# Kernel optimization log

Hardware: AMD Instinct MI355X
Metric: run time of the kernel (lower is better)

## Reference

```python
import jax, jax.numpy as jnp
import numpy as np

B, H, W, C = 2, 48, 96, 128
N = H * W
NH, HD = 8, 32
WIN_R = 1
WLEN = 2 * WIN_R + 2
ATTN_NUM = WLEN * WLEN
FIELD_DIM = 2
D_SELF = C + FIELD_DIM + NH * 2   # 146
E_SELF = D_SELF + 1               # 147 (noc embed)
D_CROSS = C + FIELD_DIM           # 130
ATTN_DIM = NH * HD                # 256
HID = C * 2                       # ConvGLU hidden
SCALE = HD ** -0.5


def init_coords():
    gx, gy = jnp.meshgrid(jnp.arange(W, dtype=jnp.float32), jnp.arange(H, dtype=jnp.float32))
    return jnp.stack([gx, gy], axis=-1)[None]  # [1,H,W,2] (x,y)


def layer_norm(x, g, b, eps=1e-5):
    mu = x.mean(-1, keepdims=True)
    var = ((x - mu) ** 2).mean(-1, keepdims=True)
    return (x - mu) * jax.lax.rsqrt(var + eps) * g + b


def swap_halves(t):
    a, b = jnp.split(t, 2, axis=0)
    return jnp.concatenate([b, a], axis=0)


def bilinear_sample(img, coords):
    # img [B,H,W,C]; coords [B,H,W,2] absolute (x,y)
    x = jnp.clip(coords[..., 0], 0.0, W - 1.0)
    y = jnp.clip(coords[..., 1], 0.0, H - 1.0)
    x0 = jnp.clip(jnp.floor(x), 0, W - 2).astype(jnp.int32); x1 = x0 + 1
    y0 = jnp.clip(jnp.floor(y), 0, H - 2).astype(jnp.int32); y1 = y0 + 1
    wx = (x - x0)[..., None]; wy = (y - y0)[..., None]
    bi = jnp.arange(img.shape[0])[:, None, None]
    v00 = img[bi, y0, x0]; v01 = img[bi, y0, x1]
    v10 = img[bi, y1, x0]; v11 = img[bi, y1, x1]
    return (1 - wy) * ((1 - wx) * v00 + wx * v01) + wy * ((1 - wx) * v10 + wx * v11)


def consistency_mask(field, A=2.0):
    offset = field + init_coords()
    f_t2r = bilinear_sample(swap_halves(field), offset)
    diff = jnp.abs(field + f_t2r).sum(-1, keepdims=True)
    return (diff < A).astype(field.dtype)  # [B,H,W,1]


def match_attention_core(q, k, v, max_offset):
    # q,k,v: [B,N,NH,HD]; max_offset: [B,N,NH,2] absolute (x,y)
    r = WIN_R
    ox = jnp.clip(max_offset[..., 0], float(r), W - 1 - r - 0.001)
    oy = jnp.clip(max_offset[..., 1], float(r), H - 1 - r - 0.001)
    mxf = jnp.floor(ox); myf = jnp.floor(oy)
    fx = (ox - mxf).transpose(0, 2, 1)[..., None, None]  # [B,NH,N,1,1]
    fy = (oy - myf).transpose(0, 2, 1)[..., None, None]
    mx = mxf.astype(jnp.int32).transpose(0, 2, 1)  # [B,NH,N]
    my = myf.astype(jnp.int32).transpose(0, 2, 1)
    qh = q.transpose(0, 2, 1, 3); kh = k.transpose(0, 2, 1, 3); vh = v.transpose(0, 2, 1, 3)
    dxs = jnp.arange(WLEN) - r                    # window: floor-r .. floor+r+1
    gx = mx[..., None] + dxs                      # [B,NH,N,WLEN]
    gy = my[..., None] + dxs
    idx = (gy[..., :, None] * W + gx[..., None, :]).reshape(B, NH, N, ATTN_NUM)
    bi = jnp.arange(B)[:, None, None, None]
    hi = jnp.arange(NH)[None, :, None, None]
    kg = kh[bi, hi, idx]                          # [B,NH,N,ATTN_NUM,HD]
    s = jnp.einsum('bhnd,bhnad->bhna', qh, kg) * SCALE
    S = s.reshape(B, NH, N, WLEN, WLEN)           # [..., y, x]
    w00 = (1 - fy) * (1 - fx); w01 = (1 - fy) * fx; w10 = fy * (1 - fx); w11 = fy * fx
    # continuous (2r+1)^2 window scores by bilinear interp of integer-grid scores
    s_cont = (w00 * S[..., :-1, :-1] + w01 * S[..., :-1, 1:]
              + w10 * S[..., 1:, :-1] + w11 * S[..., 1:, 1:])
    p = jax.nn.softmax(s_cont.reshape(B, NH, N, -1), axis=-1).reshape(s_cont.shape)
    # scatter continuous probs back to the (2r+2)^2 integer grid with bilinear weights
    Ag = jnp.zeros((B, NH, N, WLEN, WLEN), p.dtype)
    Ag = Ag.at[..., :-1, :-1].add(w00 * p)
    Ag = Ag.at[..., :-1, 1:].add(w01 * p)
    Ag = Ag.at[..., 1:, :-1].add(w10 * p)
    Ag = Ag.at[..., 1:, 1:].add(w11 * p)
    Af = Ag.reshape(B, NH, N, ATTN_NUM)
    vg = vh[bi, hi, idx]                          # [B,NH,N,ATTN_NUM,HD]
    out = jnp.einsum('bhna,bhnad->bhnd', Af, vg)
    return out.transpose(0, 2, 1, 3).reshape(B, N, ATTN_DIM), Af.transpose(0, 2, 1, 3)


def reference(x, self_rpos, field, field_scale, n0_g, n0_b, n1_g, n1_b, n2_g, n2_b,
              sq_w, sk_w, sv_w, sp_w, cq_w, ck_w, cv_w, cg_w, cp_w,
              fc1_w, fc1_b, dw_w, dw_b, fc2_w, fc2_b):
    noc = consistency_mask(jax.lax.stop_gradient(field))
    xc = jnp.concatenate([x, field * field_scale, self_rpos], axis=-1)  # [B,H,W,D_SELF]
    coords0 = jnp.tile(init_coords(), (1, 1, 1, NH))  # [1,H,W,2*NH]
    self_off = (self_rpos + coords0).reshape(B, N, NH, 2)
    # --- self MatchAttention (noc_embed) ---
    h0 = layer_norm(xc, n0_g, n0_b).reshape(B, N, D_SELF)
    xe = jnp.concatenate([h0, noc.reshape(B, N, 1)], axis=-1)
    q = (xe @ sq_w).reshape(B, N, NH, HD)
    k = (xe @ sk_w).reshape(B, N, NH, HD)
    v = (xe @ sv_w).reshape(B, N, NH, HD)
    o, _ = match_attention_core(q, k, v, self_off)
    xc = xc + (o @ sp_w).reshape(B, H, W, D_SELF)
    self_rpos_out = xc[..., -NH * 2:]
    xc = xc[..., :D_CROSS]
    xc = xc.at[..., -1].set(0.0)  # stereo: zero y-flow
    field1 = xc[..., -FIELD_DIM:] / field_scale
    off = (jnp.tile(field1, (1, 1, 1, NH)) + coords0).reshape(B, N, NH, 2)
    # --- cross MatchAttention ---
    h1 = layer_norm(xc, n1_g, n1_b).reshape(B, N, D_CROSS)
    ref = h1
    tgt = swap_halves(h1)
    g = jax.nn.silu(ref @ cg_w)
    q = (ref @ cq_w).reshape(B, N, NH, HD)
    k = (tgt @ ck_w).reshape(B, N, NH, HD)
    v = (tgt @ cv_w).reshape(B, N, NH, HD)
    o, attn = match_attention_core(q, k, v, off)
    o = jnp.concatenate([g * o, attn.reshape(B, N, NH * ATTN_NUM)], axis=-1)
    xc = xc + (o @ cp_w).reshape(B, H, W, D_CROSS)
    xc = xc.at[..., -1].set(0.0)
    field2 = xc[..., -FIELD_DIM:] / field_scale
    xo = xc[..., :C]
    # --- ConvGLU MLP ---
    h2 = layer_norm(xo, n2_g, n2_b)
    u = h2 @ fc1_w + fc1_b
    a, gv = jnp.split(u, 2, axis=-1)
    a = jax.lax.conv_general_dilated(a, dw_w, (1, 1), 'SAME',
                                     dimension_numbers=('NHWC', 'HWIO', 'NHWC'),
                                     feature_group_count=HID) + dw_b
    a = jax.nn.gelu(a, approximate=False) * gv
    xo = xo + (a @ fc2_w + fc2_b)
    return xo, self_rpos_out, field2


def setup_inputs() -> dict:
    key = jax.random.key(0)
    ks = jax.random.split(key, 16)
    def rn(i, shape, s=1.0):
        return jax.random.normal(ks[i], shape, dtype=jnp.float32) * s
    return {
        'x': rn(0, (B, H, W, C)),
        'self_rpos': rn(1, (B, H, W, NH * 2)),
        'field': rn(2, (B, H, W, FIELD_DIM)),
        'field_scale': 0.1 * jnp.ones((1, 1, 1, 2), jnp.float32),
        'n0_g': jnp.ones((D_SELF,), jnp.float32), 'n0_b': jnp.zeros((D_SELF,), jnp.float32),
        'n1_g': jnp.ones((D_CROSS,), jnp.float32), 'n1_b': jnp.zeros((D_CROSS,), jnp.float32),
        'n2_g': jnp.ones((C,), jnp.float32), 'n2_b': jnp.zeros((C,), jnp.float32),
        'sq_w': rn(3, (E_SELF, ATTN_DIM), 0.02), 'sk_w': rn(4, (E_SELF, ATTN_DIM), 0.02),
        'sv_w': rn(5, (E_SELF, ATTN_DIM), 0.02), 'sp_w': rn(6, (ATTN_DIM, D_SELF), 0.02),
        'cq_w': rn(7, (D_CROSS, ATTN_DIM), 0.02), 'ck_w': rn(8, (D_CROSS, ATTN_DIM), 0.02),
        'cv_w': rn(9, (D_CROSS, ATTN_DIM), 0.02), 'cg_w': rn(10, (D_CROSS, ATTN_DIM), 0.02),
        'cp_w': rn(11, (ATTN_DIM + NH * ATTN_NUM, D_CROSS), 0.02),
        'fc1_w': rn(12, (C, 2 * HID), 0.02), 'fc1_b': jnp.zeros((2 * HID,), jnp.float32),
        'dw_w': rn(13, (3, 3, 1, HID), 0.1), 'dw_b': jnp.zeros((HID,), jnp.float32),
        'fc2_w': rn(14, (HID, C), 0.02), 'fc2_b': jnp.zeros((C,), jnp.float32),
    }
```

## Files before the change

### kernel.cpp

```cpp
#include <hip/hip_runtime.h>
#include <math.h>

namespace {
constexpr int Bn = 2, Hh = 48, Ww = 96, Cch = 128;
constexpr int Nn = Hh * Ww;
constexpr int NHh = 8;
constexpr int DSELF = 146, ESELF = 147, DCROSS = 130;
constexpr int Mrows = Bn * Nn;
constexpr float SCALEf = 0.17677669529663687f;
}

typedef float f32x4 __attribute__((ext_vector_type(4)));
typedef short s16x8 __attribute__((ext_vector_type(8)));

__device__ __forceinline__ unsigned short f2b(float f) {
  unsigned int u = __float_as_uint(f);
  u = u + 0x7fffu + ((u >> 16) & 1u);
  return (unsigned short)(u >> 16);
}
__device__ __forceinline__ float b2f(unsigned short u) {
  return __uint_as_float((unsigned int)u << 16);
}

__device__ __forceinline__ f32x4 mfma_bf16(s16x8 a, s16x8 b, f32x4 c) {
  f32x4 d;
  asm volatile("v_mfma_f32_16x16x32_bf16 %0, %1, %2, %3"
               : "=&v"(d) : "v"(a), "v"(b), "v"(c));
  return d;
}

__device__ __forceinline__ float wave_bcast_sum(float v) {
#pragma unroll
  for (int off = 32; off > 0; off >>= 1) v += __shfl_down(v, off);
  return __shfl(v, 0);
}

struct WDesc { const float* src; int K, N, Kp, dstOff, blkOff; };
struct WPack { WDesc d[11]; };

__device__ __forceinline__ void convert_w_body(const WPack& p, unsigned short* dst,
                                               int bi) {
  int mi = 0;
#pragma unroll
  for (int i = 1; i < 11; i++) if (bi >= p.d[i].blkOff) mi = i;
  WDesc w = p.d[mi];
  int e = (bi - w.blkOff) * 2048 + threadIdx.x * 8;
  int total = w.N * w.Kp;
  if (e >= total) return;
  int n = e / w.Kp, k0 = e - n * w.Kp;
  s16x8 pack;
#pragma unroll
  for (int j = 0; j < 8; j++) {
    int kk = k0 + j;
    float vv = (kk < w.K) ? w.src[(size_t)kk * w.N + n] : 0.f;
    pack[j] = (short)f2b(vv);
  }
  *reinterpret_cast<s16x8*>(dst + w.dstOff + e) = pack;
}

__global__ __launch_bounds__(256) void mfma_gemm_kernel(
    const unsigned short* __restrict__ A, int Kp,
    const unsigned short* __restrict__ Wt, int N,
    const float* __restrict__ bias, const float* __restrict__ resid,
    void* __restrict__ out, int swapA, int act, int out_bf16) {
  __shared__ unsigned short As[64 * 40];
  __shared__ unsigned short Bs[64 * 40];
  int tid = threadIdx.x;
  int m0 = blockIdx.y * 64, n0 = blockIdx.x * 64;
  int lane = tid & 63, wv = tid >> 6;
  int wr = wv >> 1, wc = wv & 1;
  int lr = lane & 15, lk = (lane >> 4) * 8;
  int sr = tid >> 2, sk8 = (tid & 3) * 8;
  int am = m0 + sr;
  if (swapA) am = (am < Mrows / 2) ? am + Mrows / 2 : am - Mrows / 2;
  const unsigned short* aptr = A + (size_t)am * Kp + sk8;
  int bn = n0 + sr;
  const unsigned short* bptr = (bn < N) ? Wt + (size_t)bn * Kp + sk8 : nullptr;
  f32x4 acc00 = {}, acc01 = {}, acc10 = {}, acc11 = {};
  for (int k0 = 0; k0 < Kp; k0 += 32) {
    s16x8 av = *reinterpret_cast<const s16x8*>(aptr + k0);
    s16x8 bv = {};
    if (bptr) bv = *reinterpret_cast<const s16x8*>(bptr + k0);
    *reinterpret_cast<s16x8*>(&As[sr * 40 + sk8]) = av;
    *reinterpret_cast<s16x8*>(&Bs[sr * 40 + sk8]) = bv;
    __syncthreads();
    s16x8 a0 = *reinterpret_cast<const s16x8*>(&As[(wr * 32 + lr) * 40 + lk]);
    s16x8 a1 = *reinterpret_cast<const s16x8*>(&As[(wr * 32 + 16 + lr) * 40 + lk]);
    s16x8 b0 = *reinterpret_cast<const s16x8*>(&Bs[(wc * 32 + lr) * 40 + lk]);
    s16x8 b1 = *reinterpret_cast<const s16x8*>(&Bs[(wc * 32 + 16 + lr) * 40 + lk]);
    acc00 = mfma_bf16(a0, b0, acc00);
    acc01 = mfma_bf16(a0, b1, acc01);
    acc10 = mfma_bf16(a1, b0, acc10);
    acc11 = mfma_bf16(a1, b1, acc11);
    __syncthreads();
  }
  int rowBase = m0 + wr * 32 + (lane >> 4) * 4;
  f32x4 accs[2][2] = {{acc00, acc01}, {acc10, acc11}};
#pragma unroll
  for (int fc = 0; fc < 2; fc++) {
    int col = n0 + wc * 32 + fc * 16 + lr;
    if (col >= N) continue;
    float bval = bias ? bias[col] : 0.f;
    bool dosilu = (act == 1) || (act == 2 && col >= 256);
#pragma unroll
    for (int fr = 0; fr < 2; fr++) {
#pragma unroll
      for (int r = 0; r < 4; r++) {
        int row = rowBase + fr * 16 + r;
        float vv = accs[fr][fc][r] + bval;
        if (resid) vv += resid[(size_t)row * N + col];
        if (dosilu) vv = vv / (1.f + expf(-vv));
        if (out_bf16)
          ((unsigned short*)out)[(size_t)row * N + col] = f2b(vv);
        else
          ((float*)out)[(size_t)row * N + col] = vv;
      }
    }
  }
}

__global__ __launch_bounds__(128) void mfma_gemm32_kernel(
    const unsigned short* __restrict__ A, int Kp,
    const unsigned short* __restrict__ Wt, int N,
    const float* __restrict__ bias, const float* __restrict__ resid,
    void* __restrict__ out, int swapA, int act, int out_bf16) {
  __shared__ unsigned short As[32 * 40];
  __shared__ unsigned short Bs[64 * 40];
  int tid = threadIdx.x;
  int m0 = blockIdx.y * 32, n0 = blockIdx.x * 64;
  int lane = tid & 63, wv = tid >> 6;
  int lr = lane & 15, lk = (lane >> 4) * 8;
  int sr = tid >> 2, sk8 = (tid & 3) * 8;
  int am = m0 + sr;
  if (swapA) am = (am < Mrows / 2) ? am + Mrows / 2 : am - Mrows / 2;
  const unsigned short* aptr = A + (size_t)am * Kp + sk8;
  int bn0 = n0 + sr, bn1 = n0 + sr + 32;
  const unsigned short* bptr0 = (bn0 < N) ? Wt + (size_t)bn0 * Kp + sk8 : nullptr;
  const unsigned short* bptr1 = (bn1 < N) ? Wt + (size_t)bn1 * Kp + sk8 : nullptr;
  f32x4 acc00 = {}, acc01 = {}, acc10 = {}, acc11 = {};
  for (int k0 = 0; k0 < Kp; k0 += 32) {
    s16x8 av = *reinterpret_cast<const s16x8*>(aptr + k0);
    s16x8 bv0 = {}, bv1 = {};
    if (bptr0) bv0 = *reinterpret_cast<const s16x8*>(bptr0 + k0);
    if (bptr1) bv1 = *reinterpret_cast<const s16x8*>(bptr1 + k0);
    *reinterpret_cast<s16x8*>(&As[sr * 40 + sk8]) = av;
    *reinterpret_cast<s16x8*>(&Bs[sr * 40 + sk8]) = bv0;
    *reinterpret_cast<s16x8*>(&Bs[(sr + 32) * 40 + sk8]) = bv1;
    __syncthreads();
    s16x8 a0 = *reinterpret_cast<const s16x8*>(&As[lr * 40 + lk]);
    s16x8 a1 = *reinterpret_cast<const s16x8*>(&As[(16 + lr) * 40 + lk]);
    s16x8 b0 = *reinterpret_cast<const s16x8*>(&Bs[(wv * 32 + lr) * 40 + lk]);
    s16x8 b1 = *reinterpret_cast<const s16x8*>(&Bs[(wv * 32 + 16 + lr) * 40 + lk]);
    acc00 = mfma_bf16(a0, b0, acc00);
    acc01 = mfma_bf16(a0, b1, acc01);
    acc10 = mfma_bf16(a1, b0, acc10);
    acc11 = mfma_bf16(a1, b1, acc11);
    __syncthreads();
  }
  int rowBase = m0 + (lane >> 4) * 4;
  f32x4 accs[2][2] = {{acc00, acc01}, {acc10, acc11}};
#pragma unroll
  for (int fc = 0; fc < 2; fc++) {
    int col = n0 + wv * 32 + fc * 16 + lr;
    if (col >= N) continue;
    float bval = bias ? bias[col] : 0.f;
    bool dosilu = (act == 1) || (act == 2 && col >= 256);
#pragma unroll
    for (int fr = 0; fr < 2; fr++) {
#pragma unroll
      for (int r = 0; r < 4; r++) {
        int row = rowBase + fr * 16 + r;
        float vv = accs[fr][fc][r] + bval;
        if (resid) vv += resid[(size_t)row * N + col];
        if (dosilu) vv = vv / (1.f + expf(-vv));
        if (out_bf16)
          ((unsigned short*)out)[(size_t)row * N + col] = f2b(vv);
        else
          ((float*)out)[(size_t)row * N + col] = vv;
      }
    }
  }
}

__global__ __launch_bounds__(256) void prep_kernel(
    WPack wp, unsigned short* __restrict__ warena, int nconv,
    const float* __restrict__ x, const float* __restrict__ rpos,
    const float* __restrict__ field, const float* __restrict__ fs,
    const float* __restrict__ n0g, const float* __restrict__ n0b,
    float* __restrict__ xc, unsigned short* __restrict__ xe_b) {
  if (blockIdx.x < (unsigned)nconv) {
    convert_w_body(wp, warena, blockIdx.x);
    return;
  }
  int wv = threadIdx.x >> 6, lane = threadIdx.x & 63;
  int pix = (blockIdx.x - nconv) * 4 + wv;
  int b = pix / Nn, n = pix - b * Nn;
  int py = n / Ww, px = n - py * Ww;
  const float* xrow = x + (size_t)pix * Cch;
  const float* rrow = rpos + (size_t)pix * 16;
  float f0 = field[(size_t)pix * 2 + 0], f1 = field[(size_t)pix * 2 + 1];
  float fsx = fs[0], fsy = fs[1];
  float vals[3];
#pragma unroll
  for (int i = 0; i < 3; i++) {
    int c = lane + i * 64;
    float v = 0.f;
    if (c < Cch) v = xrow[c];
    else if (c == 128) v = f0 * fsx;
    else if (c == 129) v = f1 * fsy;
    else if (c < DSELF) v = rrow[c - 130];
    vals[i] = v;
  }
  float* xcrow = xc + (size_t)pix * DSELF;
#pragma unroll
  for (int i = 0; i < 3; i++) {
    int c = lane + i * 64;
    if (c < DSELF) xcrow[c] = vals[i];
  }
  float s = 0.f;
#pragma unroll
  for (int i = 0; i < 3; i++) { int c = lane + i * 64; if (c < DSELF) s += vals[i]; }
  float mu = wave_bcast_sum(s) * (1.f / DSELF);
  float s2 = 0.f;
#pragma unroll
  for (int i = 0; i < 3; i++) {
    int c = lane + i * 64;
    if (c < DSELF) { float d = vals[i] - mu; s2 += d * d; }
  }
  float var = wave_bcast_sum(s2) * (1.f / DSELF);
  float rs = rsqrtf(var + 1e-5f);
  float noc = 0.f;
  if (lane == 0) {
    float ox = fminf(fmaxf(f0 + (float)px, 0.f), (float)(Ww - 1));
    float oy = fminf(fmaxf(f1 + (float)py, 0.f), (float)(Hh - 1));
    float x0f = fminf(fmaxf(floorf(ox), 0.f), (float)(Ww - 2));
    float y0f = fminf(fmaxf(floorf(oy), 0.f), (float)(Hh - 2));
    int x0 = (int)x0f, y0 = (int)y0f;
    float wx = ox - x0f, wy = oy - y0f;
    const float* fo = field + (size_t)(1 - b) * Nn * 2;
    const float* p00 = fo + ((size_t)y0 * Ww + x0) * 2;
    const float* p10 = fo + ((size_t)(y0 + 1) * Ww + x0) * 2;
    float v0 = (1.f - wy) * ((1.f - wx) * p00[0] + wx * p00[2]) +
               wy * ((1.f - wx) * p10[0] + wx * p10[2]);
    float v1 = (1.f - wy) * ((1.f - wx) * p00[1] + wx * p00[3]) +
               wy * ((1.f - wx) * p10[1] + wx * p10[3]);
    float diff = fabsf(f0 + v0) + fabsf(f1 + v1);
    noc = (diff < 2.f) ? 1.f : 0.f;
  }
  noc = __shfl(noc, 0);
  unsigned short* xerow = xe_b + (size_t)pix * 160;
#pragma unroll
  for (int i = 0; i < 3; i++) {
    int c = lane + i * 64;
    if (c < 160) {
      float v;
      if (c < DSELF) v = (vals[i] - mu) * rs * n0g[c] + n0b[c];
      else if (c == 146) v = noc;
      else v = 0.f;
      xerow[c] = f2b(v);
    }
  }
}

__global__ __launch_bounds__(256) void attn_wave_kernel(
    const float* __restrict__ qbuf, int qstride, int gOff,
    const float* __restrict__ kvbuf, int kvstride, int koff, int voff,
    const float* __restrict__ rpos, const float* __restrict__ xc2,
    const float* __restrict__ fs, unsigned short* __restrict__ o, int o_stride,
    int mode) {
  int wv = threadIdx.x >> 6, lane = threadIdx.x & 63;
  int pix = blockIdx.x * 4 + wv;
  int b = pix / Nn, n = pix - b * Nn;
  int py = n / Ww, px = n - py * Ww;
  int h = lane >> 3, c = lane & 7;
  size_t row = (size_t)pix;
  float ox, oy;
  if (mode == 0) {
    ox = rpos[row * 16 + 2 * h] + (float)px;
    oy = rpos[row * 16 + 2 * h + 1] + (float)py;
  } else {
    ox = xc2[row * DCROSS + 128] / fs[0] + (float)px;
    oy = (float)py;
  }
  ox = fminf(fmaxf(ox, 1.0f), 93.999f);
  oy = fminf(fmaxf(oy, 1.0f), 45.999f);
  float mxf = floorf(ox), myf = floorf(oy);
  float fx = ox - mxf, fy = oy - myf;
  int mx = (int)mxf, my = (int)myf;
  int base = b * Nn;

  float4 qv = *reinterpret_cast<const float4*>(qbuf + row * qstride + lane * 4);
  float s[16];
#pragma unroll
  for (int j = 0; j < 4; j++) {
    int gy = my - 1 + j;
#pragma unroll
    for (int i = 0; i < 4; i++) {
      int gx = mx - 1 + i;
      int idx = gy * Ww + gx;
      float4 kv = *reinterpret_cast<const float4*>(
          kvbuf + (size_t)(base + idx) * kvstride + koff + lane * 4);
      float d = qv.x * kv.x + qv.y * kv.y + qv.z * kv.z + qv.w * kv.w;
      d += __shfl_xor(d, 1);
      d += __shfl_xor(d, 2);
      d += __shfl_xor(d, 4);
      s[j * 4 + i] = d * SCALEf;
    }
  }
  float w00 = (1.f - fy) * (1.f - fx), w01 = (1.f - fy) * fx;
  float w10 = fy * (1.f - fx), w11 = fy * fx;
  float sc[9];
#pragma unroll
  for (int j = 0; j < 3; j++)
#pragma unroll
    for (int i = 0; i < 3; i++)
      sc[j * 3 + i] = w00 * s[j * 4 + i] + w01 * s[j * 4 + i + 1] +
                      w10 * s[(j + 1) * 4 + i] + w11 * s[(j + 1) * 4 + i + 1];
  float mval = sc[0];
#pragma unroll
  for (int i = 1; i < 9; i++) mval = fmaxf(mval, sc[i]);
  float p[9], psum = 0.f;
#pragma unroll
  for (int i = 0; i < 9; i++) { p[i] = expf(sc[i] - mval); psum += p[i]; }
  float inv = 1.f / psum;
#pragma unroll
  for (int i = 0; i < 9; i++) p[i] *= inv;
  float Ag[16] = {};
#pragma unroll
  for (int j = 0; j < 3; j++)
#pragma unroll
    for (int i = 0; i < 3; i++) {
      float pv = p[j * 3 + i];
      Ag[j * 4 + i] += w00 * pv;
      Ag[j * 4 + i + 1] += w01 * pv;
      Ag[(j + 1) * 4 + i] += w10 * pv;
      Ag[(j + 1) * 4 + i + 1] += w11 * pv;
    }
  float4 acc = make_float4(0.f, 0.f, 0.f, 0.f);
#pragma unroll
  for (int j = 0; j < 4; j++) {
    int gy = my - 1 + j;
#pragma unroll
    for (int i = 0; i < 4; i++) {
      int gx = mx - 1 + i;
      int idx = gy * Ww + gx;
      float4 vv = *reinterpret_cast<const float4*>(
          kvbuf + (size_t)(base + idx) * kvstride + voff + lane * 4);
      float w = Ag[j * 4 + i];
      acc.x += w * vv.x; acc.y += w * vv.y; acc.z += w * vv.z; acc.w += w * vv.w;
    }
  }
  if (gOff >= 0) {
    float4 gg = *reinterpret_cast<const float4*>(qbuf + row * qstride + gOff + lane * 4);
    acc.x *= gg.x; acc.y *= gg.y; acc.z *= gg.z; acc.w *= gg.w;
  }
  unsigned int p0 = (unsigned int)f2b(acc.x) | ((unsigned int)f2b(acc.y) << 16);
  unsigned int p1 = (unsigned int)f2b(acc.z) | ((unsigned int)f2b(acc.w) << 16);
  *reinterpret_cast<uint2*>(o + row * o_stride + lane * 4) = make_uint2(p0, p1);
  if (mode == 1) {
    float a0 = 0.f, a1 = 0.f;
#pragma unroll
    for (int a = 0; a < 8; a++) {
      if (c == a) { a0 = Ag[2 * a]; a1 = Ag[2 * a + 1]; }
    }
    unsigned int pa = (unsigned int)f2b(a0) | ((unsigned int)f2b(a1) << 16);
    *reinterpret_cast<unsigned int*>(o + row * o_stride + 256 + h * 16 + 2 * c) = pa;
  }
}

__global__ __launch_bounds__(256) void post_self_kernel(
    const float* __restrict__ xcn, const float* __restrict__ n1g,
    const float* __restrict__ n1b, float* __restrict__ out_rpos,
    float* __restrict__ xc2, unsigned short* __restrict__ h1_b) {
  int wv = threadIdx.x >> 6, lane = threadIdx.x & 63;
  int pix = blockIdx.x * 4 + wv;
  const float* row = xcn + (size_t)pix * DSELF;
  float vals[3];
#pragma unroll
  for (int i = 0; i < 3; i++) {
    int c = lane + i * 64;
    vals[i] = (c < DSELF) ? row[c] : 0.f;
  }
#pragma unroll
  for (int i = 0; i < 3; i++) {
    int c = lane + i * 64;
    if (c >= 130 && c < 146) out_rpos[(size_t)pix * 16 + (c - 130)] = vals[i];
  }
#pragma unroll
  for (int i = 0; i < 3; i++) {
    int c = lane + i * 64;
    if (c == 129) vals[i] = 0.f;
  }
  float* x2row = xc2 + (size_t)pix * DCROSS;
#pragma unroll
  for (int i = 0; i < 3; i++) {
    int c = lane + i * 64;
    if (c < DCROSS) x2row[c] = vals[i];
  }
  float s = 0.f;
#pragma unroll
  for (int i = 0; i < 3; i++) { int c = lane + i * 64; if (c < DCROSS) s += vals[i]; }
  float mu = wave_bcast_sum(s) * (1.f / DCROSS);
  float s2 = 0.f;
#pragma unroll
  for (int i = 0; i < 3; i++) {
    int c = lane + i * 64;
    if (c < DCROSS) { float d = vals[i] - mu; s2 += d * d; }
  }
  float var = wave_bcast_sum(s2) * (1.f / DCROSS);
  float rs = rsqrtf(var + 1e-5f);
  unsigned short* h1row = h1_b + (size_t)pix * 160;
#pragma unroll
  for (int i = 0; i < 3; i++) {
    int c = lane + i * 64;
    if (c < 160) {
      float v = (c < DCROSS) ? (vals[i] - mu) * rs * n1g[c] + n1b[c] : 0.f;
      h1row[c] = f2b(v);
    }
  }
}

__global__ __launch_bounds__(256) void post_cross_kernel(
    const float* __restrict__ xc2n, const float* __restrict__ fs,
    const float* __restrict__ n2g, const float* __restrict__ n2b,
    float* __restrict__ out_f2, float* __restrict__ xob,
    unsigned short* __restrict__ h2_b) {
  int wv = threadIdx.x >> 6, lane = threadIdx.x & 63;
  int pix = blockIdx.x * 4 + wv;
  const float* row = xc2n + (size_t)pix * DCROSS;
  float vals[3];
#pragma unroll
  for (int i = 0; i < 3; i++) {
    int c = lane + i * 64;
    vals[i] = (c < DCROSS) ? row[c] : 0.f;
  }
  if (lane == 0) out_f2[(size_t)pix * 2 + 0] = vals[2] / fs[0];
  if (lane == 1) out_f2[(size_t)pix * 2 + 1] = 0.f;
  float* xrow = xob + (size_t)pix * Cch;
#pragma unroll
  for (int i = 0; i < 2; i++) {
    int c = lane + i * 64;
    xrow[c] = vals[i];
  }
  float s = vals[0] + vals[1];
  float mu = wave_bcast_sum(s) * (1.f / Cch);
  float d0 = vals[0] - mu, d1 = vals[1] - mu;
  float var = wave_bcast_sum(d0 * d0 + d1 * d1) * (1.f / Cch);
  float rs = rsqrtf(var + 1e-5f);
  unsigned short* h2row = h2_b + (size_t)pix * Cch;
#pragma unroll
  for (int i = 0; i < 2; i++) {
    int c = lane + i * 64;
    h2row[c] = f2b((vals[i] - mu) * rs * n2g[c] + n2b[c]);
  }
}

__global__ __launch_bounds__(256) void dwconv_kernel(
    const unsigned short* __restrict__ ub, const float* __restrict__ dww,
    const float* __restrict__ dwb, unsigned short* __restrict__ aout) {
  int t = blockIdx.x * 256 + threadIdx.x;
  int c8 = (t & 31) * 8;
  int pix = t >> 5;
  int b = pix / Nn, n = pix - b * Nn;
  int py = n / Ww, px = n - py * Ww;
  float acc[8];
#pragma unroll
  for (int j = 0; j < 8; j++) acc[j] = dwb[c8 + j];
#pragma unroll
  for (int ky = 0; ky < 3; ky++) {
    int yy = py + ky - 1;
    if (yy < 0 || yy >= Hh) continue;
#pragma unroll
    for (int kx = 0; kx < 3; kx++) {
      int xx = px + kx - 1;
      if (xx < 0 || xx >= Ww) continue;
      s16x8 uv = *reinterpret_cast<const s16x8*>(
          ub + ((size_t)(b * Nn + yy * Ww + xx)) * 512 + c8);
      const float* wrow = dww + (ky * 3 + kx) * 256 + c8;
#pragma unroll
      for (int j = 0; j < 8; j++)
        acc[j] += b2f((unsigned short)uv[j]) * wrow[j];
    }
  }
  s16x8 gate = *reinterpret_cast<const s16x8*>(ub + (size_t)pix * 512 + 256 + c8);
  s16x8 outp;
#pragma unroll
  for (int j = 0; j < 8; j++) {
    float a = acc[j];
    float ge = 0.5f * a * (1.f + erff(a * 0.70710678118654752f));
    outp[j] = (short)f2b(ge * b2f((unsigned short)gate[j]));
  }
  *reinterpret_cast<s16x8*>(aout + (size_t)pix * 256 + c8) = outp;
}

extern "C" void kernel_launch(void* const* d_in, const int* in_sizes, int n_in,
                              void* d_out, int out_size, void* d_ws, size_t ws_size,
                              hipStream_t stream) {
  (void)in_sizes; (void)n_in; (void)out_size; (void)ws_size;
  const float* x    = (const float*)d_in[0];
  const float* rpos = (const float*)d_in[1];
  const float* field= (const float*)d_in[2];
  const float* fs   = (const float*)d_in[3];
  const float* n0g  = (const float*)d_in[4];
  const float* n0b  = (const float*)d_in[5];
  const float* n1g  = (const float*)d_in[6];
  const float* n1b  = (const float*)d_in[7];
  const float* n2g  = (const float*)d_in[8];
  const float* n2b  = (const float*)d_in[9];
  const float* sq_w = (const float*)d_in[10];
  const float* sk_w = (const float*)d_in[11];
  const float* sv_w = (const float*)d_in[12];
  const float* sp_w = (const float*)d_in[13];
  const float* cq_w = (const float*)d_in[14];
  const float* ck_w = (const float*)d_in[15];
  const float* cv_w = (const float*)d_in[16];
  const float* cg_w = (const float*)d_in[17];
  const float* cp_w = (const float*)d_in[18];
  const float* fc1w = (const float*)d_in[19];
  const float* fc1b = (const float*)d_in[20];
  const float* dww  = (const float*)d_in[21];
  const float* dwb  = (const float*)d_in[22];
  const float* fc2w = (const float*)d_in[23];
  const float* fc2b = (const float*)d_in[24];

  float* ws = (float*)d_ws;
  float* xc    = ws + 0;
  float* xcn   = ws + 1345536;
  float* xc2   = ws + 2691072;
  float* xc2n  = ws + 3889152;
  float* xob   = ws + 5087232;
  unsigned short* xe_b   = (unsigned short*)(ws + 6266880);
  unsigned short* h1_b   = (unsigned short*)(ws + 7004160);
  unsigned short* h2_b   = (unsigned short*)(ws + 7741440);
  float* qkv   = ws + 8331264;
  float* qg    = ws + 15409152;
  float* kv    = ws + 20127744;
  unsigned short* o_b    = (unsigned short*)(ws + 24846336);
  unsigned short* ocat_b = (unsigned short*)(ws + 26025984);
  unsigned short* warena = (unsigned short*)(ws + 27795456);
  unsigned short* u_b    = (unsigned short*)qkv;
  unsigned short* aconv_b = o_b;

  float* out_xo   = (float*)d_out;
  float* out_rpos = out_xo + 1179648;
  float* out_f2   = out_xo + 1327104;

  const int oSQKV = 0;
  const int oSP   = 122880;
  const int oCQG  = 160256;
  const int oCKV  = 242176;
  const int oCP   = 324096;
  const int oF1   = 374016;
  const int oF2   = 439552;
  WPack wp;
  auto setw = [&](int i, const float* src, int K, int N, int Kp, int off) {
    wp.d[i].src = src; wp.d[i].K = K; wp.d[i].N = N; wp.d[i].Kp = Kp;
    wp.d[i].dstOff = off;
  };
  setw(0, sq_w, 147, 256, 160, oSQKV);
  setw(1, sk_w, 147, 256, 160, oSQKV + 40960);
  setw(2, sv_w, 147, 256, 160, oSQKV + 81920);
  setw(3, sp_w, 256, 146, 256, oSP);
  setw(4, cq_w, 130, 256, 160, oCQG);
  setw(5, cg_w, 130, 256, 160, oCQG + 40960);
  setw(6, ck_w, 130, 256, 160, oCKV);
  setw(7, cv_w, 130, 256, 160, oCKV + 40960);
  setw(8, cp_w, 384, 130, 384, oCP);
  setw(9, fc1w, 128, 512, 128, oF1);
  setw(10, fc2w, 256, 128, 256, oF2);
  int nblk = 0;
  for (int i = 0; i < 11; i++) {
    wp.d[i].blkOff = nblk;
    nblk += (wp.d[i].N * wp.d[i].Kp + 2047) / 2048;
  }

  dim3 blk(256);
  auto gemm = [&](const unsigned short* A, int Kp, int woff, int N,
                  const float* bias, const float* resid, void* out,
                  int swapA, int act, int obf) {
    if (N <= 384) {
      dim3 grid((N + 63) / 64, Mrows / 32);
      mfma_gemm32_kernel<<<grid, dim3(128), 0, stream>>>(
          A, Kp, warena + woff, N, bias, resid, out, swapA, act, obf);
    } else {
      dim3 grid((N + 63) / 64, Mrows / 64);
      mfma_gemm_kernel<<<grid, blk, 0, stream>>>(
          A, Kp, warena + woff, N, bias, resid, out, swapA, act, obf);
    }
  };

  prep_kernel<<<nblk + 2304, blk, 0, stream>>>(wp, warena, nblk, x, rpos, field,
                                               fs, n0g, n0b, xc, xe_b);
  gemm(xe_b, 160, oSQKV, 768, nullptr, nullptr, qkv, 0, 0, 0);
  attn_wave_kernel<<<2304, blk, 0, stream>>>(qkv, 768, -1, qkv, 768, 256, 512,
                                             rpos, nullptr, fs, o_b, 256, 0);
  gemm(o_b, 256, oSP, 146, nullptr, xc, xcn, 0, 0, 0);
  post_self_kernel<<<2304, blk, 0, stream>>>(xcn, n1g, n1b, out_rpos, xc2, h1_b);
  gemm(h1_b, 160, oCQG, 512, nullptr, nullptr, qg, 0, 2, 0);
  gemm(h1_b, 160, oCKV, 512, nullptr, nullptr, kv, 1, 0, 0);
  attn_wave_kernel<<<2304, blk, 0, stream>>>(qg, 512, 256, kv, 512, 0, 256,
                                             nullptr, xc2, fs, ocat_b, 384, 1);
  gemm(ocat_b, 384, oCP, 130, nullptr, xc2, xc2n, 0, 0, 0);
  post_cross_kernel<<<2304, blk, 0, stream>>>(xc2n, fs, n2g, n2b, out_f2, xob, h2_b);
  gemm(h2_b, 128, oF1, 512, fc1b, nullptr, u_b, 0, 0, 1);
  dwconv_kernel<<<1152, blk, 0, stream>>>(u_b, dww, dwb, aconv_b);
  gemm(aconv_b, 256, oF2, 128, fc2b, xob, out_xo, 0, 0, 0);
}
```

Before: 160.9 us.

## Store attention K/V in fp16 and merge cross Q/G and K/V GEMMs

Measured after the change: 147.7 us, median of 2. 8.2% less time.

```diff
diff --git a/kernel.cpp b/kernel.cpp
--- a/kernel.cpp
+++ b/kernel.cpp
@@ -12,6 +12,7 @@
 
 typedef float f32x4 __attribute__((ext_vector_type(4)));
 typedef short s16x8 __attribute__((ext_vector_type(8)));
+typedef _Float16 h16x4 __attribute__((ext_vector_type(4)));
 
 __device__ __forceinline__ unsigned short f2b(float f) {
   unsigned int u = __float_as_uint(f);
@@ -20,6 +21,10 @@
 }
 __device__ __forceinline__ float b2f(unsigned short u) {
   return __uint_as_float((unsigned int)u << 16);
+}
+__device__ __forceinline__ float4 ld4h(const _Float16* p) {
+  h16x4 h = *reinterpret_cast<const h16x4*>(p);
+  return make_float4((float)h[0], (float)h[1], (float)h[2], (float)h[3]);
 }
 
 __device__ __forceinline__ f32x4 mfma_bf16(s16x8 a, s16x8 b, f32x4 c) {
@@ -58,11 +63,31 @@
   *reinterpret_cast<s16x8*>(dst + w.dstOff + e) = pack;
 }
 
+__device__ __forceinline__ void gemm_store(
+    float vv, int row, int col, int N, int colSplit,
+    const float* __restrict__ bias, const float* __restrict__ resid,
+    void* __restrict__ out0, void* __restrict__ out1, int mode0, int act) {
+  if (bias) vv += bias[col];
+  if (act == 1 || (act == 3 && col >= 256 && col < 512))
+    vv = vv / (1.f + expf(-vv));
+  if (col < colSplit) {
+    if (resid) vv += resid[(size_t)row * colSplit + col];
+    if (mode0)
+      ((unsigned short*)out0)[(size_t)row * colSplit + col] = f2b(vv);
+    else
+      ((float*)out0)[(size_t)row * colSplit + col] = vv;
+  } else {
+    ((_Float16*)out1)[(size_t)row * (N - colSplit) + (col - colSplit)] =
+        (_Float16)vv;
+  }
+}
+
 __global__ __launch_bounds__(256) void mfma_gemm_kernel(
     const unsigned short* __restrict__ A, int Kp,
     const unsigned short* __restrict__ Wt, int N,
     const float* __restrict__ bias, const float* __restrict__ resid,
-    void* __restrict__ out, int swapA, int act, int out_bf16) {
+    void* __restrict__ out0, void* __restrict__ out1, int colSplit,
+    int mode0, int swapMode, int act) {
   __shared__ unsigned short As[64 * 40];
   __shared__ unsigned short Bs[64 * 40];
   int tid = threadIdx.x;
@@ -72,7 +97,8 @@
   int lr = lane & 15, lk = (lane >> 4) * 8;
   int sr = tid >> 2, sk8 = (tid & 3) * 8;
   int am = m0 + sr;
-  if (swapA) am = (am < Mrows / 2) ? am + Mrows / 2 : am - Mrows / 2;
+  int swp = (swapMode == 1) || (swapMode == 2 && n0 >= colSplit);
+  if (swp) am = (am < Mrows / 2) ? am + Mrows / 2 : am - Mrows / 2;
   const unsigned short* aptr = A + (size_t)am * Kp + sk8;
   int bn = n0 + sr;
   const unsigned short* bptr = (bn < N) ? Wt + (size_t)bn * Kp + sk8 : nullptr;
@@ -100,20 +126,13 @@
   for (int fc = 0; fc < 2; fc++) {
     int col = n0 + wc * 32 + fc * 16 + lr;
     if (col >= N) continue;
-    float bval = bias ? bias[col] : 0.f;
-    bool dosilu = (act == 1) || (act == 2 && col >= 256);
 #pragma unroll
     for (int fr = 0; fr < 2; fr++) {
 #pragma unroll
       for (int r = 0; r < 4; r++) {
         int row = rowBase + fr * 16 + r;
-        float vv = accs[fr][fc][r] + bval;
-        if (resid) vv += resid[(size_t)row * N + col];
-        if (dosilu) vv = vv / (1.f + expf(-vv));
-        if (out_bf16)
-          ((unsigned short*)out)[(size_t)row * N + col] = f2b(vv);
-        else
-          ((float*)out)[(size_t)row * N + col] = vv;
+        gemm_store(accs[fr][fc][r], row, col, N, colSplit, bias, resid,
+                   out0, out1, mode0, act);
       }
     }
   }
@@ -123,7 +142,8 @@
     const unsigned short* __restrict__ A, int Kp,
     const unsigned short* __restrict__ Wt, int N,
     const float* __restrict__ bias, const float* __restrict__ resid,
-    void* __restrict__ out, int swapA, int act, int out_bf16) {
+    void* __restrict__ out0, void* __restrict__ out1, int colSplit,
+    int mode0, int swapMode, int act) {
   __shared__ unsigned short As[32 * 40];
   __shared__ unsigned short Bs[64 * 40];
   int tid = threadIdx.x;
@@ -132,7 +152,8 @@
   int lr = lane & 15, lk = (lane >> 4) * 8;
   int sr = tid >> 2, sk8 = (tid & 3) * 8;
   int am = m0 + sr;
-  if (swapA) am = (am < Mrows / 2) ? am + Mrows / 2 : am - Mrows / 2;
+  int swp = (swapMode == 1) || (swapMode == 2 && n0 >= colSplit);
+  if (swp) am = (am < Mrows / 2) ? am + Mrows / 2 : am - Mrows / 2;
   const unsigned short* aptr = A + (size_t)am * Kp + sk8;
   int bn0 = n0 + sr, bn1 = n0 + sr + 32;
   const unsigned short* bptr0 = (bn0 < N) ? Wt + (size_t)bn0 * Kp + sk8 : nullptr;
@@ -163,20 +184,13 @@
   for (int fc = 0; fc < 2; fc++) {
     int col = n0 + wv * 32 + fc * 16 + lr;
     if (col >= N) continue;
-    float bval = bias ? bias[col] : 0.f;
-    bool dosilu = (act == 1) || (act == 2 && col >= 256);
 #pragma unroll
     for (int fr = 0; fr < 2; fr++) {
 #pragma unroll
       for (int r = 0; r < 4; r++) {
         int row = rowBase + fr * 16 + r;
-        float vv = accs[fr][fc][r] + bval;
-        if (resid) vv += resid[(size_t)row * N + col];
-        if (dosilu) vv = vv / (1.f + expf(-vv));
-        if (out_bf16)
-          ((unsigned short*)out)[(size_t)row * N + col] = f2b(vv);
-        else
-          ((float*)out)[(size_t)row * N + col] = vv;
+        gemm_store(accs[fr][fc][r], row, col, N, colSplit, bias, resid,
+                   out0, out1, mode0, act);
       }
     }
   }
@@ -264,7 +278,7 @@
 
 __global__ __launch_bounds__(256) void attn_wave_kernel(
     const float* __restrict__ qbuf, int qstride, int gOff,
-    const float* __restrict__ kvbuf, int kvstride, int koff, int voff,
+    const _Float16* __restrict__ kvbuf,
     const float* __restrict__ rpos, const float* __restrict__ xc2,
     const float* __restrict__ fs, unsigned short* __restrict__ o, int o_stride,
     int mode) {
@@ -298,8 +312,7 @@
     for (int i = 0; i < 4; i++) {
       int gx = mx - 1 + i;
       int idx = gy * Ww + gx;
-      float4 kv = *reinterpret_cast<const float4*>(
-          kvbuf + (size_t)(base + idx) * kvstride + koff + lane * 4);
+      float4 kv = ld4h(kvbuf + (size_t)(base + idx) * 512 + lane * 4);
       float d = qv.x * kv.x + qv.y * kv.y + qv.z * kv.z + qv.w * kv.w;
       d += __shfl_xor(d, 1);
       d += __shfl_xor(d, 2);
@@ -344,8 +357,7 @@
     for (int i = 0; i < 4; i++) {
       int gx = mx - 1 + i;
       int idx = gy * Ww + gx;
-      float4 vv = *reinterpret_cast<const float4*>(
-          kvbuf + (size_t)(base + idx) * kvstride + voff + lane * 4);
+      float4 vv = ld4h(kvbuf + (size_t)(base + idx) * 512 + 256 + lane * 4);
       float w = Ag[j * 4 + i];
       acc.x += w * vv.x; acc.y += w * vv.y; acc.z += w * vv.z; acc.w += w * vv.w;
     }
@@ -529,16 +541,16 @@
   float* xc2   = ws + 2691072;
   float* xc2n  = ws + 3889152;
   float* xob   = ws + 5087232;
-  unsigned short* xe_b   = (unsigned short*)(ws + 6266880);
-  unsigned short* h1_b   = (unsigned short*)(ws + 7004160);
-  unsigned short* h2_b   = (unsigned short*)(ws + 7741440);
-  float* qkv   = ws + 8331264;
-  float* qg    = ws + 15409152;
-  float* kv    = ws + 20127744;
-  unsigned short* o_b    = (unsigned short*)(ws + 24846336);
-  unsigned short* ocat_b = (unsigned short*)(ws + 26025984);
-  unsigned short* warena = (unsigned short*)(ws + 27795456);
-  unsigned short* u_b    = (unsigned short*)qkv;
+  unsigned short* xe_b = (unsigned short*)(ws + 6266880);
+  unsigned short* h1_b = (unsigned short*)(ws + 7004160);
+  unsigned short* h2_b = (unsigned short*)(ws + 7741440);
+  float* q32   = ws + 8331264;
+  _Float16* kv16 = (_Float16*)(ws + 10690560);
+  float* qg    = ws + 13049856;
+  unsigned short* o_b    = (unsigned short*)(ws + 17768448);
+  unsigned short* ocat_b = (unsigned short*)(ws + 18948096);
+  unsigned short* warena = (unsigned short*)(ws + 20717568);
+  unsigned short* u_b    = (unsigned short*)qg;
   unsigned short* aconv_b = o_b;
 
   float* out_xo   = (float*)d_out;
@@ -547,8 +559,7 @@
 
   const int oSQKV = 0;
   const int oSP   = 122880;
-  const int oCQG  = 160256;
-  const int oCKV  = 242176;
+  const int oCQGKV= 160256;
   const int oCP   = 324096;
   const int oF1   = 374016;
   const int oF2   = 439552;
@@ -561,10 +572,10 @@
   setw(1, sk_w, 147, 256, 160, oSQKV + 40960);
   setw(2, sv_w, 147, 256, 160, oSQKV + 81920);
   setw(3, sp_w, 256, 146, 256, oSP);
-  setw(4, cq_w, 130, 256, 160, oCQG);
-  setw(5, cg_w, 130, 256, 160, oCQG + 40960);
-  setw(6, ck_w, 130, 256, 160, oCKV);
-  setw(7, cv_w, 130, 256, 160, oCKV + 40960);
+  setw(4, cq_w, 130, 256, 160, oCQGKV);
+  setw(5, cg_w, 130, 256, 160, oCQGKV + 40960);
+  setw(6, ck_w, 130, 256, 160, oCQGKV + 81920);
+  setw(7, cv_w, 130, 256, 160, oCQGKV + 122880);
   setw(8, cp_w, 384, 130, 384, oCP);
   setw(9, fc1w, 128, 512, 128, oF1);
   setw(10, fc2w, 256, 128, 256, oF2);
@@ -576,33 +587,34 @@
 
   dim3 blk(256);
   auto gemm = [&](const unsigned short* A, int Kp, int woff, int N,
-                  const float* bias, const float* resid, void* out,
-                  int swapA, int act, int obf) {
+                  const float* bias, const float* resid, void* out0, void* out1,
+                  int colSplit, int mode0, int swapMode, int act) {
     if (N <= 384) {
       dim3 grid((N + 63) / 64, Mrows / 32);
       mfma_gemm32_kernel<<<grid, dim3(128), 0, stream>>>(
-          A, Kp, warena + woff, N, bias, resid, out, swapA, act, obf);
+          A, Kp, warena + woff, N, bias, resid, out0, out1, colSplit, mode0,
+          swapMode, act);
     } else {
       dim3 grid((N + 63) / 64, Mrows / 64);
       mfma_gemm_kernel<<<grid, blk, 0, stream>>>(
-          A, Kp, warena + woff, N, bias, resid, out, swapA, act, obf);
+          A, Kp, warena + woff, N, bias, resid, out0, out1, colSplit, mode0,
+          swapMode, act);
     }
   };
 
   prep_kernel<<<nblk + 2304, blk, 0, stream>>>(wp, warena, nblk, x, rpos, field,
                                                fs, n0g, n0b, xc, xe_b);
-  gemm(xe_b, 160, oSQKV, 768, nullptr, nullptr, qkv, 0, 0, 0);
-  attn_wave_kernel<<<2304, blk, 0, stream>>>(qkv, 768, -1, qkv, 768, 256, 512,
-                                             rpos, nullptr, fs, o_b, 256, 0);
-  gemm(o_b, 256, oSP, 146, nullptr, xc, xcn, 0, 0, 0);
+  gemm(xe_b, 160, oSQKV, 768, nullptr, nullptr, q32, kv16, 256, 0, 0, 0);
+  attn_wave_kernel<<<2304, blk, 0, stream>>>(q32, 256, -1, kv16, rpos, nullptr,
+                                             fs, o_b, 256, 0);
+  gemm(o_b, 256, oSP, 146, nullptr, xc, xcn, nullptr, 146, 0, 0, 0);
   post_self_kernel<<<2304, blk, 0, stream>>>(xcn, n1g, n1b, out_rpos, xc2, h1_b);
-  gemm(h1_b, 160, oCQG, 512, nullptr, nullptr, qg, 0, 2, 0);
-  gemm(h1_b, 160, oCKV, 512, nullptr, nullptr, kv, 1, 0, 0);
-  attn_wave_kernel<<<2304, blk, 0, stream>>>(qg, 512, 256, kv, 512, 0, 256,
-                                             nullptr, xc2, fs, ocat_b, 384, 1);
-  gemm(ocat_b, 384, oCP, 130, nullptr, xc2, xc2n, 0, 0, 0);
+  gemm(h1_b, 160, oCQGKV, 1024, nullptr, nullptr, qg, kv16, 512, 0, 2, 3);
+  attn_wave_kernel<<<2304, blk, 0, stream>>>(qg, 512, 256, kv16, nullptr, xc2,
+                                             fs, ocat_b, 384, 1);
+  gemm(ocat_b, 384, oCP, 130, nullptr, xc2, xc2n, nullptr, 130, 0, 0, 0);
   post_cross_kernel<<<2304, blk, 0, stream>>>(xc2n, fs, n2g, n2b, out_f2, xob, h2_b);
-  gemm(h2_b, 128, oF1, 512, fc1b, nullptr, u_b, 0, 0, 1);
+  gemm(h2_b, 128, oF1, 512, fc1b, nullptr, u_b, nullptr, 512, 1, 0, 0);
   dwconv_kernel<<<1152, blk, 0, stream>>>(u_b, dww, dwb, aconv_b);
-  gemm(aconv_b, 256, oF2, 128, fc2b, xob, out_xo, 0, 0, 0);
-}
+  gemm(aconv_b, 256, oF2, 128, fc2b, xob, out_xo, nullptr, 128, 0, 0, 0);
+}
```
